# Optimization experiments

Measured on AMD Instinct MI355X. Metric: run time of the kernel, lower is better.

## Reference

```python
import jax, jax.numpy as jnp
import numpy as np

B, T, IN, H, OUT = 128, 512, 64, 512, 1
H2 = H // 2


def setup_inputs() -> dict:
    key = jax.random.key(0)
    ks = jax.random.split(key, 16)
    s_in = 1.0 / np.sqrt(H)  # torch LSTM/Linear init scale ~ U(-1/sqrt(H), 1/sqrt(H))
    def u(k, shape, s):
        return jax.random.uniform(k, shape, jnp.float32, -s, s)
    return {
        "x": jax.random.normal(ks[0], (B, T, IN), jnp.float32),
        "W_ih0": u(ks[1], (4 * H, IN), s_in),
        "W_hh0": u(ks[2], (4 * H, H), s_in),
        "b_ih0": u(ks[3], (4 * H,), s_in),
        "b_hh0": u(ks[4], (4 * H,), s_in),
        "W_ih1": u(ks[5], (4 * H, H), s_in),
        "W_hh1": u(ks[6], (4 * H, H), s_in),
        "b_ih1": u(ks[7], (4 * H,), s_in),
        "b_hh1": u(ks[8], (4 * H,), s_in),
        "fc1_w": u(ks[9], (H2, H), s_in),
        "fc1_b": u(ks[10], (H2,), s_in),
        "fc2_w": u(ks[11], (OUT, H2), 1.0 / np.sqrt(H2)),
        "fc2_b": u(ks[12], (OUT,), 1.0 / np.sqrt(H2)),
    }


def _lstm_layer(x, W_ih, W_hh, b_ih, b_hh):
    # x: [B, T, D_in] -> outputs h for all timesteps [B, T, H]
    b, t, _ = x.shape
    h_dim = W_hh.shape[1]
    # precompute input contribution to gates for all timesteps: [T, B, 4H]
    xg = (jnp.einsum('btd,gd->btg', x, W_ih) + b_ih + b_hh).transpose(1, 0, 2)

    def step(carry, xt):
        h, c = carry
        gates = xt + h @ W_hh.T  # [B, 4H]
        i, f, g, o = jnp.split(gates, 4, axis=-1)  # torch gate order i,f,g,o
        i = jax.nn.sigmoid(i)
        f = jax.nn.sigmoid(f)
        g = jnp.tanh(g)
        o = jax.nn.sigmoid(o)
        c = f * c + i * g
        h = o * jnp.tanh(c)
        return (h, c), h

    h0 = jnp.zeros((b, h_dim), x.dtype)
    (_, _), hs = jax.lax.scan(step, (h0, h0), xg)
    return hs.transpose(1, 0, 2)  # [B, T, H]


def reference(x, W_ih0, W_hh0, b_ih0, b_hh0, W_ih1, W_hh1, b_ih1, b_hh1,
              fc1_w, fc1_b, fc2_w, fc2_b):
    h1 = _lstm_layer(x, W_ih0, W_hh0, b_ih0, b_hh0)
    h2 = _lstm_layer(h1, W_ih1, W_hh1, b_ih1, b_hh1)
    last = h2[:, -1, :]  # [B, H]
    z = jax.nn.relu(last @ fc1_w.T + fc1_b)
    return z @ fc2_w.T + fc2_b  # [B, OUT]
```

## Files before the change

kernel.cpp:

```cpp
#include <hip/hip_runtime.h>
#include <hip/hip_fp16.h>

#define BB   128
#define TT   512
#define INS  64
#define HH   512
#define K0   576
#define K1   1024
#define PAD0 584
#define PAD1 1032
#define NWG  128
#define NTHR 512
#define H2   256

typedef _Float16 f16;
typedef f16 f16x4 __attribute__((ext_vector_type(4)));
typedef f16 f16x8 __attribute__((ext_vector_type(8)));
typedef float f32x4 __attribute__((ext_vector_type(4)));

__device__ __forceinline__ float sigmoidf_(float x) {
  return 1.0f / (1.0f + __expf(-x));
}
__device__ __forceinline__ float tanhf_(float x) {
  return 1.0f - 2.0f / (__expf(2.0f * x) + 1.0f);
}

__global__ __launch_bounds__(NTHR, 1) void lstm_fused(
    const float* __restrict__ x,
    const float* __restrict__ Wih0, const float* __restrict__ Whh0,
    const float* __restrict__ bih0, const float* __restrict__ bhh0,
    const float* __restrict__ Wih1, const float* __restrict__ Whh1,
    const float* __restrict__ bih1, const float* __restrict__ bhh1,
    int* __restrict__ bar, f16* __restrict__ h1buf, f16* __restrict__ h2buf)
{
  extern __shared__ f16 smem[];
  f16* W0s = smem;
  f16* W1s = smem + 32 * PAD0;

  const int tid  = threadIdx.x;
  const int wg   = blockIdx.x;
  const int mg   = wg >> 6;
  const int ng   = wg & 63;
  const int wid  = tid >> 6;
  const int lane = tid & 63;

  for (int e4 = tid; e4 < 32 * (K0 / 4); e4 += NTHR) {
    int r = e4 / (K0 / 4), k = (e4 - r * (K0 / 4)) * 4;
    int g = ((r >> 3) << 9) + (ng << 3) + (r & 7);
    float4 v = (k < INS)
        ? *reinterpret_cast<const float4*>(Wih0 + g * INS + k)
        : *reinterpret_cast<const float4*>(Whh0 + g * HH + (k - INS));
    f16x4 h; h[0]=(f16)v.x; h[1]=(f16)v.y; h[2]=(f16)v.z; h[3]=(f16)v.w;
    *reinterpret_cast<f16x4*>(&W0s[r * PAD0 + k]) = h;
  }
  for (int e4 = tid; e4 < 32 * (K1 / 4); e4 += NTHR) {
    int r = e4 >> 8, k = (e4 & 255) * 4;
    int g = ((r >> 3) << 9) + (ng << 3) + (r & 7);
    float4 v = (k < HH)
        ? *reinterpret_cast<const float4*>(Wih1 + g * HH + k)
        : *reinterpret_cast<const float4*>(Whh1 + g * HH + (k - HH));
    f16x4 h; h[0]=(f16)v.x; h[1]=(f16)v.y; h[2]=(f16)v.z; h[3]=(f16)v.w;
    *reinterpret_cast<f16x4*>(&W1s[r * PAD1 + k]) = h;
  }

  const bool isL1 = (wid >= 4);
  const int  wrow = mg * 64 + (wid & 3) * 16;
  const int  col0 = lane & 15;
  const int  rA   = lane & 15;
  const int  kq   = (lane >> 4) * 8;
  const int  hcol = (ng << 3) + (lane & 7);
  const bool low  = (lane & 8) == 0;

  float bias[2];
  #pragma unroll
  for (int n = 0; n < 2; n++) {
    int c = n * 16 + col0;
    int g = ((c >> 3) << 9) + (ng << 3) + (c & 7);
    bias[n] = isL1 ? (bih1[g] + bhh1[g]) : (bih0[g] + bhh0[g]);
  }
  __syncthreads();

  f32x4 cst = {};

  int* grp  = bar + (wg & 7) * 64;
  int* glob = bar + 512;
  int* genp = bar + 576;

  for (int s = 0; s <= TT; ++s) {
    const f16* h1r = h1buf + ((s + 1) & 1) * (BB * HH);
    f16*       h1w = h1buf + ((s    ) & 1) * (BB * HH);
    const f16* h2r = h2buf + ((s    ) & 1) * (BB * HH);
    f16*       h2w = h2buf + ((s + 1) & 1) * (BB * HH);

    const bool active = isL1 ? (s >= 1) : (s < TT);
    if (active) {
      const int row = wrow + rA;
      f32x4 acc0 = {}, acc1 = {};

      if (!isL1) {
        const float* xb = x + ((size_t)row * TT + (size_t)s) * INS;
        #pragma unroll
        for (int ks = 0; ks < 2; ++ks) {
          const int kk = ks * 32 + kq;
          float4 q0 = *reinterpret_cast<const float4*>(xb + kk);
          float4 q1 = *reinterpret_cast<const float4*>(xb + kk + 4);
          f16x8 a;
          a[0]=(f16)q0.x; a[1]=(f16)q0.y; a[2]=(f16)q0.z; a[3]=(f16)q0.w;
          a[4]=(f16)q1.x; a[5]=(f16)q1.y; a[6]=(f16)q1.z; a[7]=(f16)q1.w;
          f16x8 b0 = *reinterpret_cast<const f16x8*>(&W0s[col0 * PAD0 + kk]);
          f16x8 b1 = *reinterpret_cast<const f16x8*>(&W0s[(16 + col0) * PAD0 + kk]);
          acc0 = __builtin_amdgcn_mfma_f32_16x16x32_f16(a, b0, acc0, 0, 0, 0);
          acc1 = __builtin_amdgcn_mfma_f32_16x16x32_f16(a, b1, acc1, 0, 0, 0);
        }
        #pragma unroll
        for (int c = 0; c < 2; ++c) {
          f16x8 a[8];
          #pragma unroll
          for (int u = 0; u < 8; ++u) {
            const int kh = (c * 8 + u) * 32 + kq;
            a[u] = *reinterpret_cast<const f16x8*>(h1r + row * HH + kh);
          }
          #pragma unroll
          for (int u = 0; u < 8; ++u) {
            const int kk = INS + (c * 8 + u) * 32 + kq;
            f16x8 b0 = *reinterpret_cast<const f16x8*>(&W0s[col0 * PAD0 + kk]);
            f16x8 b1 = *reinterpret_cast<const f16x8*>(&W0s[(16 + col0) * PAD0 + kk]);
            acc0 = __builtin_amdgcn_mfma_f32_16x16x32_f16(a[u], b0, acc0, 0, 0, 0);
            acc1 = __builtin_amdgcn_mfma_f32_16x16x32_f16(a[u], b1, acc1, 0, 0, 0);
          }
        }
      } else {
        #pragma unroll
        for (int c = 0; c < 4; ++c) {
          f16x8 a[8];
          #pragma unroll
          for (int u = 0; u < 8; ++u) {
            const int kk = (c * 8 + u) * 32 + kq;
            a[u] = (c < 2)
                ? *reinterpret_cast<const f16x8*>(h1r + row * HH + kk)
                : *reinterpret_cast<const f16x8*>(h2r + row * HH + (kk - HH));
          }
          #pragma unroll
          for (int u = 0; u < 8; ++u) {
            const int kk = (c * 8 + u) * 32 + kq;
            f16x8 b0 = *reinterpret_cast<const f16x8*>(&W1s[col0 * PAD1 + kk]);
            f16x8 b1 = *reinterpret_cast<const f16x8*>(&W1s[(16 + col0) * PAD1 + kk]);
            acc0 = __builtin_amdgcn_mfma_f32_16x16x32_f16(a[u], b0, acc0, 0, 0, 0);
            acc1 = __builtin_amdgcn_mfma_f32_16x16x32_f16(a[u], b1, acc1, 0, 0, 0);
          }
        }
      }

      float res[4];
      #pragma unroll
      for (int j = 0; j < 4; j++) {
        float v0 = acc0[j] + bias[0];
        float v1 = acc1[j] + bias[1];
        float p0 = __shfl_xor(v0, 8, 64);
        float p1 = __shfl_xor(v1, 8, 64);
        float ip = low ? v0 : p0;
        float fp = low ? p0 : v0;
        float gp = low ? v1 : p1;
        float op = low ? p1 : v1;
        float cn = sigmoidf_(fp) * cst[j] + sigmoidf_(ip) * tanhf_(gp);
        cst[j] = cn;
        res[j] = sigmoidf_(op) * tanhf_(cn);
      }
      if (low) {
        f16* hw = isL1 ? h2w : h1w;
        const int rowb = wrow + ((lane >> 4) << 2);
        #pragma unroll
        for (int j = 0; j < 4; j++)
          hw[(rowb + j) * HH + hcol] = (f16)res[j];
      }
    }

    __syncthreads();
    if (tid == 0) {
      int gen = __hip_atomic_load(genp, __ATOMIC_RELAXED, __HIP_MEMORY_SCOPE_AGENT);
      int p = __hip_atomic_fetch_add(grp, 1, __ATOMIC_ACQ_REL, __HIP_MEMORY_SCOPE_AGENT);
      if (p == 15) {
        __hip_atomic_store(grp, 0, __ATOMIC_RELAXED, __HIP_MEMORY_SCOPE_AGENT);
        int q = __hip_atomic_fetch_add(glob, 1, __ATOMIC_ACQ_REL, __HIP_MEMORY_SCOPE_AGENT);
        if (q == 7) {
          __hip_atomic_store(glob, 0, __ATOMIC_RELAXED, __HIP_MEMORY_SCOPE_AGENT);
          __hip_atomic_fetch_add(genp, 1, __ATOMIC_RELEASE, __HIP_MEMORY_SCOPE_AGENT);
        }
      }
      while (__hip_atomic_load(genp, __ATOMIC_RELAXED, __HIP_MEMORY_SCOPE_AGENT) == gen)
        __builtin_amdgcn_s_sleep(1);
      (void)__hip_atomic_load(genp, __ATOMIC_ACQUIRE, __HIP_MEMORY_SCOPE_AGENT);
    }
    __syncthreads();
  }
}

__global__ void fc1_kernel(const f16* __restrict__ last, const float* __restrict__ w,
                           const float* __restrict__ b, float* __restrict__ z) {
  const int bb = blockIdx.x;
  const int j  = threadIdx.x;
  const f16*   lp = last + bb * HH;
  const float* wp = w + j * HH;
  float s = b[j];
  #pragma unroll 8
  for (int k = 0; k < HH; k++) s += (float)lp[k] * wp[k];
  z[bb * H2 + j] = fmaxf(s, 0.0f);
}

__global__ void fc2_kernel(const float* __restrict__ z, const float* __restrict__ w,
                           const float* __restrict__ b, float* __restrict__ out) {
  const int bb = threadIdx.x;
  float s = b[0];
  #pragma unroll 8
  for (int k = 0; k < H2; k++) s += z[bb * H2 + k] * w[k];
  out[bb] = s;
}

extern "C" void kernel_launch(void* const* d_in, const int* in_sizes, int n_in,
                              void* d_out, int out_size, void* d_ws, size_t ws_size,
                              hipStream_t stream) {
  const float* x     = (const float*)d_in[0];
  const float* Wih0  = (const float*)d_in[1];
  const float* Whh0  = (const float*)d_in[2];
  const float* bih0  = (const float*)d_in[3];
  const float* bhh0  = (const float*)d_in[4];
  const float* Wih1  = (const float*)d_in[5];
  const float* Whh1  = (const float*)d_in[6];
  const float* bih1  = (const float*)d_in[7];
  const float* bhh1  = (const float*)d_in[8];
  const float* fc1w  = (const float*)d_in[9];
  const float* fc1b  = (const float*)d_in[10];
  const float* fc2w  = (const float*)d_in[11];
  const float* fc2b  = (const float*)d_in[12];

  char* ws = (char*)d_ws;
  int*  bar = (int*)ws;
  f16*  h1  = (f16*)(ws + 4096);
  f16*  h2  = h1 + 2 * BB * HH;
  float* z  = (float*)(ws + 4096 + (size_t)4 * BB * HH * sizeof(f16));

  hipMemsetAsync(ws, 0, 4096 + (size_t)4 * BB * HH * sizeof(f16), stream);

  const size_t smem = (size_t)(32 * PAD0 + 32 * PAD1) * sizeof(f16);
  lstm_fused<<<NWG, NTHR, smem, stream>>>(x, Wih0, Whh0, bih0, bhh0,
                                          Wih1, Whh1, bih1, bhh1, bar, h1, h2);

  const f16* last = h2 + ((TT - 1) & 1) * (BB * HH);
  fc1_kernel<<<BB, 256, 0, stream>>>(last, fc1w, fc1b, z);
  fc2_kernel<<<1, BB, 0, stream>>>(z, fc2w, fc2b, (float*)d_out);
}
```

Before: 7.166 ms.

## Split grid barrier per batch half and use relaxed coherent loads/stores

The single grid-wide barrier becomes two independent barriers, one per 64-row batch half (mg), since each half only depends on its own rows. Monotonic counters compared against the step index replace the counter resets, and acquire/release atomics are dropped. Hidden-state exchange now uses relaxed agent-scope atomic loads and packed 32-bit stores, plus an explicit vmcnt wait before the barrier, so L2-coherent traffic replaces the cache flushes that acq_rel implied. Correctness depends on relaxed atomics plus waitcnt giving enough visibility across workgroups without explicit fences.

```diff
diff --git a/kernel.cpp b/kernel.cpp
--- a/kernel.cpp
+++ b/kernel.cpp
@@ -25,6 +25,17 @@
   return 1.0f - 2.0f / (__expf(2.0f * x) + 1.0f);
 }
 
+__device__ __forceinline__ f16x8 ldg_h(const f16* p) {
+  union { unsigned long long q[2]; f16x8 v; } u;
+  const unsigned long long* qp = (const unsigned long long*)p;
+  u.q[0] = __hip_atomic_load(qp,     __ATOMIC_RELAXED, __HIP_MEMORY_SCOPE_AGENT);
+  u.q[1] = __hip_atomic_load(qp + 1, __ATOMIC_RELAXED, __HIP_MEMORY_SCOPE_AGENT);
+  return u.v;
+}
+__device__ __forceinline__ void stg_h(f16* p, unsigned int pk) {
+  __hip_atomic_store((unsigned int*)p, pk, __ATOMIC_RELAXED, __HIP_MEMORY_SCOPE_AGENT);
+}
+
 __global__ __launch_bounds__(NTHR, 1) void lstm_fused(
     const float* __restrict__ x,
     const float* __restrict__ Wih0, const float* __restrict__ Whh0,
@@ -70,6 +81,7 @@
   const int  kq   = (lane >> 4) * 8;
   const int  hcol = (ng << 3) + (lane & 7);
   const bool low  = (lane & 8) == 0;
+  const bool evn  = (lane & 1) == 0;
 
   float bias[2];
   #pragma unroll
@@ -82,9 +94,10 @@
 
   f32x4 cst = {};
 
-  int* grp  = bar + (wg & 7) * 64;
-  int* glob = bar + 512;
-  int* genp = bar + 576;
+  int* barh = bar + mg * 1024;
+  int* grp  = barh + (ng & 7) * 64;
+  int* glob = barh + 512;
+  int* genp = barh + 576;
 
   for (int s = 0; s <= TT; ++s) {
     const f16* h1r = h1buf + ((s + 1) & 1) * (BB * HH);
@@ -118,7 +131,7 @@
           #pragma unroll
           for (int u = 0; u < 8; ++u) {
             const int kh = (c * 8 + u) * 32 + kq;
-            a[u] = *reinterpret_cast<const f16x8*>(h1r + row * HH + kh);
+            a[u] = ldg_h(h1r + row * HH + kh);
           }
           #pragma unroll
           for (int u = 0; u < 8; ++u) {
@@ -136,9 +149,8 @@
           #pragma unroll
           for (int u = 0; u < 8; ++u) {
             const int kk = (c * 8 + u) * 32 + kq;
-            a[u] = (c < 2)
-                ? *reinterpret_cast<const f16x8*>(h1r + row * HH + kk)
-                : *reinterpret_cast<const f16x8*>(h2r + row * HH + (kk - HH));
+            a[u] = (c < 2) ? ldg_h(h1r + row * HH + kk)
+                           : ldg_h(h2r + row * HH + (kk - HH));
           }
           #pragma unroll
           for (int u = 0; u < 8; ++u) {
@@ -166,30 +178,35 @@
         cst[j] = cn;
         res[j] = sigmoidf_(op) * tanhf_(cn);
       }
-      if (low) {
+      {
         f16* hw = isL1 ? h2w : h1w;
         const int rowb = wrow + ((lane >> 4) << 2);
         #pragma unroll
-        for (int j = 0; j < 4; j++)
-          hw[(rowb + j) * HH + hcol] = (f16)res[j];
+        for (int j = 0; j < 4; j++) {
+          float other = __shfl_xor(res[j], 1, 64);
+          if (low && evn) {
+            f16 lo_ = (f16)res[j], hi_ = (f16)other;
+            unsigned int pk =
+                (unsigned int)__builtin_bit_cast(unsigned short, lo_) |
+                ((unsigned int)__builtin_bit_cast(unsigned short, hi_) << 16);
+            stg_h(hw + (rowb + j) * HH + hcol, pk);
+          }
+        }
       }
     }
 
+    asm volatile("s_waitcnt vmcnt(0)" ::: "memory");
     __syncthreads();
     if (tid == 0) {
-      int gen = __hip_atomic_load(genp, __ATOMIC_RELAXED, __HIP_MEMORY_SCOPE_AGENT);
-      int p = __hip_atomic_fetch_add(grp, 1, __ATOMIC_ACQ_REL, __HIP_MEMORY_SCOPE_AGENT);
-      if (p == 15) {
-        __hip_atomic_store(grp, 0, __ATOMIC_RELAXED, __HIP_MEMORY_SCOPE_AGENT);
-        int q = __hip_atomic_fetch_add(glob, 1, __ATOMIC_ACQ_REL, __HIP_MEMORY_SCOPE_AGENT);
-        if (q == 7) {
-          __hip_atomic_store(glob, 0, __ATOMIC_RELAXED, __HIP_MEMORY_SCOPE_AGENT);
-          __hip_atomic_fetch_add(genp, 1, __ATOMIC_RELEASE, __HIP_MEMORY_SCOPE_AGENT);
-        }
-      }
-      while (__hip_atomic_load(genp, __ATOMIC_RELAXED, __HIP_MEMORY_SCOPE_AGENT) == gen)
+      int p = __hip_atomic_fetch_add(grp, 1, __ATOMIC_RELAXED, __HIP_MEMORY_SCOPE_AGENT);
+      if ((p & 7) == 7) {
+        int q = __hip_atomic_fetch_add(glob, 1, __ATOMIC_RELAXED, __HIP_MEMORY_SCOPE_AGENT);
+        if ((q & 7) == 7)
+          __hip_atomic_fetch_add(genp, 1, __ATOMIC_RELAXED, __HIP_MEMORY_SCOPE_AGENT);
+      }
+      while (__hip_atomic_load(genp, __ATOMIC_RELAXED, __HIP_MEMORY_SCOPE_AGENT) < s + 1)
         __builtin_amdgcn_s_sleep(1);
-      (void)__hip_atomic_load(genp, __ATOMIC_ACQUIRE, __HIP_MEMORY_SCOPE_AGENT);
+      asm volatile("" ::: "memory");
     }
     __syncthreads();
   }
@@ -235,11 +252,11 @@
 
   char* ws = (char*)d_ws;
   int*  bar = (int*)ws;
-  f16*  h1  = (f16*)(ws + 4096);
+  f16*  h1  = (f16*)(ws + 8192);
   f16*  h2  = h1 + 2 * BB * HH;
-  float* z  = (float*)(ws + 4096 + (size_t)4 * BB * HH * sizeof(f16));
-
-  hipMemsetAsync(ws, 0, 4096 + (size_t)4 * BB * HH * sizeof(f16), stream);
+  float* z  = (float*)(ws + 8192 + (size_t)4 * BB * HH * sizeof(f16));
+
+  hipMemsetAsync(ws, 0, 8192 + (size_t)4 * BB * HH * sizeof(f16), stream);
 
   const size_t smem = (size_t)(32 * PAD0 + 32 * PAD1) * sizeof(f16);
   lstm_fused<<<NWG, NTHR, smem, stream>>>(x, Wih0, Whh0, bih0, bhh0,
```

New measurement: 7.286 ms. No clear change (+1.7%).
